# Kernel optimization log

Measured on AMD Instinct MI355X. Metric: run time of the kernel, lower is better.

## Reference

```python
import jax, jax.numpy as jnp
import numpy as np


def apply_rope(x):
    # x: [B, T, H, D]
    T, D = x.shape[1], x.shape[3]
    inv_freq = 1.0 / (10000.0 ** (jnp.arange(0, D, 2, dtype=jnp.float32) / D))  # [D/2]
    t = jnp.arange(T, dtype=jnp.float32)
    freqs = jnp.outer(t, inv_freq)  # [T, D/2]
    sin_f = jnp.sin(freqs)[None, :, None, :]
    cos_f = jnp.cos(freqs)[None, :, None, :]
    x1, x2 = jnp.split(x, 2, axis=-1)
    return jnp.concatenate([x1 * cos_f - x2 * sin_f, x1 * sin_f + x2 * cos_f], axis=-1)


def setup_inputs() -> dict:
    key = jax.random.key(0)
    ks = jax.random.split(key, 5)
    B, T, D = 8, 8192, 128
    s = 1.0 / np.sqrt(D)
    return {
        "x": jax.random.normal(ks[0], (B, T, D), dtype=jnp.float32),
        "Wq": jax.random.normal(ks[1], (D, D), dtype=jnp.float32) * s,
        "bq": jnp.zeros((D,), dtype=jnp.float32),
        "Wk": jax.random.normal(ks[2], (D, D), dtype=jnp.float32) * s,
        "bk": jnp.zeros((D,), dtype=jnp.float32),
        "Wv": jax.random.normal(ks[3], (D, D), dtype=jnp.float32) * s,
        "bv": jnp.zeros((D,), dtype=jnp.float32),
        "Wo": jax.random.normal(ks[4], (D, D), dtype=jnp.float32) * s,
        "bo": jnp.zeros((D,), dtype=jnp.float32),
    }


def reference(x, Wq, bq, Wk, bk, Wv, bv, Wo, bo):
    n_heads = 8
    B, T, d_model = x.shape
    head_dim = d_model // n_heads

    q = (x @ Wq + bq).reshape(B, T, n_heads, head_dim)
    k = (x @ Wk + bk).reshape(B, T, n_heads, head_dim)
    v = (x @ Wv + bv).reshape(B, T, n_heads, head_dim)

    q = jax.nn.elu(apply_rope(q)) + 1.0
    k = jax.nn.elu(apply_rope(k)) + 1.0

    # non-causal linear attention: context = sum_t k_t v_t^T per head
    context = jnp.einsum("bthd,bthe->bhde", k, v)            # [B,H,Dh,Dh]
    out = jnp.einsum("bthd,bhde->bthe", q, context)           # [B,T,H,Dh]
    k_sum = jnp.sum(k, axis=1)                                  # [B,H,Dh]
    z = 1.0 / (jnp.einsum("bthd,bhd->bth", q, k_sum) + 1e-6)  # [B,T,H]
    out = out * z[..., None]

    out = out.reshape(B, T, d_model)
    return out @ Wo + bo
```

## Files before the change

kernel.cpp:

```cpp
#include <hip/hip_runtime.h>
#include <hip/hip_bf16.h>


typedef __attribute__((ext_vector_type(8))) short short8;
typedef __attribute__((ext_vector_type(4))) float floatx4;

#define DEV __device__ __forceinline__
#define MFMA __builtin_amdgcn_mfma_f32_16x16x32_bf16

DEV unsigned short bfh(float f) {
  unsigned int x = __float_as_uint(f);
  x += 0x7fffu + ((x >> 16) & 1u);
  return (unsigned short)(x >> 16);
}
DEV float bfdec(unsigned short u) { return __uint_as_float(((unsigned int)u) << 16); }
DEV void splitf(float f, unsigned short& h, unsigned short& l) {
  h = bfh(f);
  l = bfh(f - bfdec(h));
}
DEV void split8(const float* p, short8& h8, short8& l8) {
  float4 a = *(const float4*)p;
  float4 b = *(const float4*)(p + 4);
  float v[8] = {a.x, a.y, a.z, a.w, b.x, b.y, b.z, b.w};
  union { short8 s; unsigned short u[8]; } H, L;
#pragma unroll
  for (int i = 0; i < 8; ++i) splitf(v[i], H.u[i], L.u[i]);
  h8 = H.s; l8 = L.s;
}

DEV void xpose_frag(floatx4 m0, floatx4 m1, int lane16, int quad,
                    short8& hi, short8& lo) {
  union { short8 s; unsigned short u[8]; } H, L;
#pragma unroll
  for (int j = 0; j < 8; ++j) {
    int srcLane = lane16 + (((quad & 1) * 2 + (j >> 2)) << 4);
    float vA = __shfl(m0[j & 3], srcLane, 64);
    float vB = __shfl(m1[j & 3], srcLane, 64);
    float v = (quad < 2) ? vA : vB;
    splitf(v, H.u[j], L.u[j]);
  }
  hi = H.s; lo = L.s;
}

__global__ void k_prep(const float* __restrict__ Wq, const float* __restrict__ Wk,
                       const float* __restrict__ Wv, const float* __restrict__ Wo,
                       unsigned short* __restrict__ WTh, unsigned short* __restrict__ WTl,
                       float* __restrict__ ctxz) {
  int gid = blockIdx.x * 256 + threadIdx.x;
  if (gid < 8192) {
    int mat = gid >> 11, r = gid & 2047, n = r >> 4, k0 = (r & 15) * 8;
    const float* W = (mat == 0) ? Wq : (mat == 1) ? Wk : (mat == 2) ? Wv : Wo;
    union { uint4 q; unsigned short u[8]; } oh, ol;
#pragma unroll
    for (int i = 0; i < 8; ++i) splitf(W[(size_t)(k0 + i) * 128 + n], oh.u[i], ol.u[i]);
    *(uint4*)&WTh[mat * 16384 + n * 128 + k0] = oh.q;
    *(uint4*)&WTl[mat * 16384 + n * 128 + k0] = ol.q;
  } else if (gid < 8192 + 17408) {
    ctxz[gid - 8192] = 0.0f;
  }
}

DEV void stage_rope64(int tid, int t0, float rc[64][9], float rs[64][9]) {
#pragma unroll
  for (int p = 0; p < 2; ++p) {
    int idx = tid + p * 256;
    int r = idx >> 3, j = idx & 7;
    float invf = 1.0f / powf(10000.0f, (float)j * 0.125f);
    float s, c;
    sincosf((float)(t0 + r) * invf, &s, &c);
    rc[r][j] = c; rs[r][j] = s;
  }
}

__global__ __launch_bounds__(256, 2) void k_qkv_ctx(
    const float* __restrict__ x,
    const unsigned short* __restrict__ WTh, const unsigned short* __restrict__ WTl,
    const float* __restrict__ bq, const float* __restrict__ bk, const float* __restrict__ bv,
    float* __restrict__ ctx, float* __restrict__ ksum,
    unsigned short* __restrict__ qws) {
  __shared__ float rc[64][9], rs[64][9];
  const int tid = threadIdx.x;
  const int row0 = blockIdx.x * 64;
  const int b = row0 >> 13;
  const int t0 = row0 & 8191;

  stage_rope64(tid, t0, rc, rs);
  __syncthreads();

  const int l = tid & 63, w = tid >> 6;
  const int lane16 = l & 15, quad = l >> 4;

  floatx4 acc[6][4];
#pragma unroll
  for (int i = 0; i < 6; ++i)
#pragma unroll
    for (int j = 0; j < 4; ++j) acc[i][j] = (floatx4){0.f, 0.f, 0.f, 0.f};

#pragma unroll
  for (int ks = 0; ks < 4; ++ks) {
    short8 afh[4], afl[4];
#pragma unroll
    for (int mt = 0; mt < 4; ++mt)
      split8(x + (size_t)(row0 + mt * 16 + lane16) * 128 + ks * 32 + quad * 8, afh[mt], afl[mt]);
#pragma unroll
    for (int nt = 0; nt < 6; ++nt) {
      int mat = nt >> 1;
      size_t woff = (size_t)mat * 16384 +
                    (size_t)(w * 32 + (nt & 1) * 16 + lane16) * 128 + ks * 32 + quad * 8;
      short8 bh = *(const short8*)(WTh + woff);
      short8 bl = *(const short8*)(WTl + woff);
#pragma unroll
      for (int mt = 0; mt < 4; ++mt) {
        acc[nt][mt] = MFMA(afh[mt], bh, acc[nt][mt], 0, 0, 0);
        acc[nt][mt] = MFMA(afl[mt], bh, acc[nt][mt], 0, 0, 0);
        acc[nt][mt] = MFMA(afh[mt], bl, acc[nt][mt], 0, 0, 0);
      }
    }
  }

#pragma unroll
  for (int nt = 0; nt < 6; ++nt) {
    int col = w * 32 + (nt & 1) * 16 + lane16;
    int mat = nt >> 1;
    float bias = (mat == 0) ? bq[col] : (mat == 1) ? bk[col] : bv[col];
#pragma unroll
    for (int mt = 0; mt < 4; ++mt)
#pragma unroll
      for (int r = 0; r < 4; ++r) acc[nt][mt][r] += bias;
  }

  {
    const int d = lane16, j = d & 7;
#pragma unroll
    for (int mt = 0; mt < 4; ++mt) {
      float cc[4], ss[4];
#pragma unroll
      for (int r = 0; r < 4; ++r) {
        int tl = mt * 16 + quad * 4 + r;
        cc[r] = rc[tl][j]; ss[r] = rs[tl][j];
      }
#pragma unroll
      for (int nt = 0; nt < 4; ++nt) {
#pragma unroll
        for (int r = 0; r < 4; ++r) {
          float v = acc[nt][mt][r];
          float p = __shfl_xor(v, 8);
          float nv = (d < 8) ? (v * cc[r] - p * ss[r]) : (p * ss[r] + v * cc[r]);
          acc[nt][mt][r] = (nv > 0.f) ? (nv + 1.f) : __expf(nv);
        }
      }
    }
  }

#pragma unroll
  for (int kt = 0; kt < 2; ++kt) {
    float s = 0.f;
#pragma unroll
    for (int mt = 0; mt < 4; ++mt)
#pragma unroll
      for (int r = 0; r < 4; ++r) s += acc[2 + kt][mt][r];
    s += __shfl_xor(s, 16);
    s += __shfl_xor(s, 32);
    if (l < 16) atomicAdd(&ksum[(b * 8 + w * 2 + kt) * 16 + lane16], s);
  }

#pragma unroll
  for (int qt = 0; qt < 2; ++qt) {
    int h = w * 2 + qt;
#pragma unroll
    for (int mt = 0; mt < 4; ++mt)
#pragma unroll
      for (int r = 0; r < 4; ++r)
        qws[(size_t)(row0 + mt * 16 + quad * 4 + r) * 128 + h * 16 + lane16] =
            bfh(acc[qt][mt][r]);
  }

#pragma unroll
  for (int hl = 0; hl < 2; ++hl) {
    int h = w * 2 + hl;
    floatx4 c = (floatx4){0.f, 0.f, 0.f, 0.f};
#pragma unroll
    for (int ks2 = 0; ks2 < 2; ++ks2) {
      short8 kh, kl, vh, vl;
      xpose_frag(acc[2 + hl][ks2 * 2], acc[2 + hl][ks2 * 2 + 1], lane16, quad, kh, kl);
      xpose_frag(acc[4 + hl][ks2 * 2], acc[4 + hl][ks2 * 2 + 1], lane16, quad, vh, vl);
      c = MFMA(kh, vh, c, 0, 0, 0);
      c = MFMA(kl, vh, c, 0, 0, 0);
      c = MFMA(kh, vl, c, 0, 0, 0);
    }
#pragma unroll
    for (int r = 0; r < 4; ++r)
      atomicAdd(&ctx[((size_t)(b * 8 + h) * 16 + quad * 4 + r) * 16 + lane16], c[r]);
  }
}

__global__ __launch_bounds__(256, 2) void k_apply_out(
    const unsigned short* __restrict__ qws,
    const unsigned short* __restrict__ WToh, const unsigned short* __restrict__ WTol,
    const float* __restrict__ bo,
    const float* __restrict__ ctx, const float* __restrict__ ksum,
    float* __restrict__ out) {
  __shared__ unsigned short CTh[8 * 16 * 40], CTl[8 * 16 * 40];
  __shared__ float ksumS[128], boS[128];
  const int tid = threadIdx.x;
  const int row0 = blockIdx.x * 128;
  const int b = row0 >> 13;

  if (tid < 128) {
    int h = tid >> 4, e = tid & 15, p = h & 1;
    unsigned int base = (h * 16 + e) * 40;
    union { uint4 q; unsigned int u[4]; } z0; z0.u[0] = z0.u[1] = z0.u[2] = z0.u[3] = 0;
    *(uint4*)&CTh[base + (1 - p) * 16] = z0.q;
    *(uint4*)&CTh[base + (1 - p) * 16 + 8] = z0.q;
    *(uint4*)&CTl[base + (1 - p) * 16] = z0.q;
    *(uint4*)&CTl[base + (1 - p) * 16 + 8] = z0.q;
    const float* cp = ctx + (size_t)(b * 8 + h) * 256 + e;
    union { uint4 q; unsigned short u[8]; } ch, cl;
#pragma unroll
    for (int d = 0; d < 8; ++d) splitf(cp[d * 16], ch.u[d], cl.u[d]);
    *(uint4*)&CTh[base + p * 16] = ch.q;
    *(uint4*)&CTl[base + p * 16] = cl.q;
#pragma unroll
    for (int d = 0; d < 8; ++d) splitf(cp[(8 + d) * 16], ch.u[d], cl.u[d]);
    *(uint4*)&CTh[base + p * 16 + 8] = ch.q;
    *(uint4*)&CTl[base + p * 16 + 8] = cl.q;
  } else {
    int t2 = tid - 128;
    ksumS[t2] = ksum[b * 128 + t2];
    boS[t2] = bo[t2];
  }
  __syncthreads();

  const int l = tid & 63, w = tid >> 6;
  const int lane16 = l & 15, quad = l >> 4;

  floatx4 of[2][8];
  short8 qf[2][4];
  float ziP[2][4];

#pragma unroll
  for (int mt2 = 0; mt2 < 2; ++mt2) {
    int trow = row0 + w * 32 + mt2 * 16 + lane16;
#pragma unroll
    for (int hp = 0; hp < 4; ++hp)
      qf[mt2][hp] = *(const short8*)&qws[(size_t)trow * 128 + hp * 32 + quad * 8];
#pragma unroll
    for (int hp = 0; hp < 4; ++hp) {
      union { short8 s8; unsigned short u[8]; } qq; qq.s8 = qf[mt2][hp];
      float s = 0.f;
#pragma unroll
      for (int jj = 0; jj < 8; ++jj)
        s += bfdec(qq.u[jj]) * ksumS[hp * 32 + quad * 8 + jj];
      s += __shfl_xor(s, 16);
      ziP[mt2][hp] = 1.0f / (s + 1e-6f);
    }
#pragma unroll
    for (int h = 0; h < 8; ++h) {
      int ca = (h * 16 + lane16) * 40 + quad * 8;
      short8 avh = *(const short8*)&CTh[ca];
      short8 avl = *(const short8*)&CTl[ca];
      floatx4 o = (floatx4){0.f, 0.f, 0.f, 0.f};
      o = MFMA(avh, qf[mt2][h >> 1], o, 0, 0, 0);
      o = MFMA(avl, qf[mt2][h >> 1], o, 0, 0, 0);
      float zz = __shfl(ziP[mt2][h >> 1], ((h & 1) << 5) + lane16, 64);
#pragma unroll
      for (int r = 0; r < 4; ++r) of[mt2][h][r] = o[r] * zz;
    }
  }

  short8 oah[2][4], oal[2][4];
#pragma unroll
  for (int mt2 = 0; mt2 < 2; ++mt2)
#pragma unroll
    for (int ksx = 0; ksx < 4; ++ksx)
      xpose_frag(of[mt2][ksx * 2], of[mt2][ksx * 2 + 1], lane16, quad, oah[mt2][ksx], oal[mt2][ksx]);

  floatx4 oacc[2][8];
#pragma unroll
  for (int i = 0; i < 2; ++i)
#pragma unroll
    for (int j = 0; j < 8; ++j) oacc[i][j] = (floatx4){0.f, 0.f, 0.f, 0.f};

#pragma unroll
  for (int nt = 0; nt < 8; ++nt) {
#pragma unroll
    for (int ks = 0; ks < 4; ++ks) {
      size_t off = (size_t)(nt * 16 + lane16) * 128 + ks * 32 + quad * 8;
      short8 wbh = *(const short8*)(WToh + off);
      short8 wbl = *(const short8*)(WTol + off);
#pragma unroll
      for (int mt2 = 0; mt2 < 2; ++mt2) {
        oacc[mt2][nt] = MFMA(oah[mt2][ks], wbh, oacc[mt2][nt], 0, 0, 0);
        oacc[mt2][nt] = MFMA(oal[mt2][ks], wbh, oacc[mt2][nt], 0, 0, 0);
        oacc[mt2][nt] = MFMA(oah[mt2][ks], wbl, oacc[mt2][nt], 0, 0, 0);
      }
    }
  }

#pragma unroll
  for (int nt = 0; nt < 8; ++nt) {
    int oc = nt * 16 + lane16;
    float bb = boS[oc];
#pragma unroll
    for (int mt2 = 0; mt2 < 2; ++mt2)
#pragma unroll
      for (int r = 0; r < 4; ++r) {
        int t = row0 + w * 32 + mt2 * 16 + quad * 4 + r;
        out[(size_t)t * 128 + oc] = oacc[mt2][nt][r] + bb;
      }
  }
}

extern "C" void kernel_launch(void* const* d_in, const int* in_sizes, int n_in,
                              void* d_out, int out_size, void* d_ws, size_t ws_size,
                              hipStream_t stream) {
  const float* x  = (const float*)d_in[0];
  const float* Wq = (const float*)d_in[1];
  const float* bq = (const float*)d_in[2];
  const float* Wk = (const float*)d_in[3];
  const float* bk = (const float*)d_in[4];
  const float* Wv = (const float*)d_in[5];
  const float* bv = (const float*)d_in[6];
  const float* Wo = (const float*)d_in[7];
  const float* bo = (const float*)d_in[8];
  float* out = (float*)d_out;

  unsigned short* qws = (unsigned short*)d_ws;
  unsigned short* WTh = qws + 8388608;
  unsigned short* WTl = WTh + 65536;
  float* ctx  = (float*)(WTl + 65536);
  float* ksum = ctx + 16384;

  k_prep<<<100, 256, 0, stream>>>(Wq, Wk, Wv, Wo, WTh, WTl, ctx);
  k_qkv_ctx<<<1024, 256, 0, stream>>>(x, WTh, WTl, bq, bk, bv, ctx, ksum, qws);
  k_apply_out<<<512, 256, 0, stream>>>(qws, WTh + 3 * 16384, WTl + 3 * 16384,
                                       bo, ctx, ksum, out);
}
```

Before: 172.3 us.

## Fold context into Wo per batch and stage split x in LDS with 512 threads

```diff
diff --git a/kernel.cpp b/kernel.cpp
--- a/kernel.cpp
+++ b/kernel.cpp
@@ -43,56 +43,62 @@
 }
 
 __global__ void k_prep(const float* __restrict__ Wq, const float* __restrict__ Wk,
-                       const float* __restrict__ Wv, const float* __restrict__ Wo,
+                       const float* __restrict__ Wv,
                        unsigned short* __restrict__ WTh, unsigned short* __restrict__ WTl,
                        float* __restrict__ ctxz) {
   int gid = blockIdx.x * 256 + threadIdx.x;
-  if (gid < 8192) {
+  if (gid < 6144) {
     int mat = gid >> 11, r = gid & 2047, n = r >> 4, k0 = (r & 15) * 8;
-    const float* W = (mat == 0) ? Wq : (mat == 1) ? Wk : (mat == 2) ? Wv : Wo;
+    const float* W = (mat == 0) ? Wq : (mat == 1) ? Wk : Wv;
     union { uint4 q; unsigned short u[8]; } oh, ol;
 #pragma unroll
     for (int i = 0; i < 8; ++i) splitf(W[(size_t)(k0 + i) * 128 + n], oh.u[i], ol.u[i]);
     *(uint4*)&WTh[mat * 16384 + n * 128 + k0] = oh.q;
     *(uint4*)&WTl[mat * 16384 + n * 128 + k0] = ol.q;
-  } else if (gid < 8192 + 17408) {
-    ctxz[gid - 8192] = 0.0f;
-  }
-}
-
-DEV void stage_rope64(int tid, int t0, float rc[64][9], float rs[64][9]) {
-#pragma unroll
-  for (int p = 0; p < 2; ++p) {
-    int idx = tid + p * 256;
-    int r = idx >> 3, j = idx & 7;
-    float invf = 1.0f / powf(10000.0f, (float)j * 0.125f);
-    float s, c;
-    sincosf((float)(t0 + r) * invf, &s, &c);
-    rc[r][j] = c; rs[r][j] = s;
-  }
-}
-
-__global__ __launch_bounds__(256, 2) void k_qkv_ctx(
+  } else if (gid < 6144 + 17408) {
+    ctxz[gid - 6144] = 0.0f;
+  }
+}
+
+__global__ __launch_bounds__(512) void k_qkv(
     const float* __restrict__ x,
     const unsigned short* __restrict__ WTh, const unsigned short* __restrict__ WTl,
     const float* __restrict__ bq, const float* __restrict__ bk, const float* __restrict__ bv,
     float* __restrict__ ctx, float* __restrict__ ksum,
     unsigned short* __restrict__ qws) {
+  __shared__ unsigned short xh[64 * 136], xl[64 * 136];
   __shared__ float rc[64][9], rs[64][9];
   const int tid = threadIdx.x;
   const int row0 = blockIdx.x * 64;
   const int b = row0 >> 13;
   const int t0 = row0 & 8191;
 
-  stage_rope64(tid, t0, rc, rs);
+  {
+    int r = tid >> 3, j = tid & 7;
+    float invf = 1.0f / powf(10000.0f, (float)j * 0.125f);
+    float s, c;
+    sincosf((float)(t0 + r) * invf, &s, &c);
+    rc[r][j] = c; rs[r][j] = s;
+  }
+  {
+    int r = tid >> 3, cg = (tid & 7) * 16;
+    const float* xp = x + (size_t)(row0 + r) * 128 + cg;
+    short8 h0, l0, h1, l1;
+    split8(xp, h0, l0);
+    split8(xp + 8, h1, l1);
+    *(short8*)&xh[r * 136 + cg] = h0;
+    *(short8*)&xh[r * 136 + cg + 8] = h1;
+    *(short8*)&xl[r * 136 + cg] = l0;
+    *(short8*)&xl[r * 136 + cg + 8] = l1;
+  }
   __syncthreads();
 
   const int l = tid & 63, w = tid >> 6;
   const int lane16 = l & 15, quad = l >> 4;
 
-  floatx4 acc[6][4];
-#pragma unroll
-  for (int i = 0; i < 6; ++i)
+  floatx4 acc[3][4];
+#pragma unroll
+  for (int i = 0; i < 3; ++i)
 #pragma unroll
     for (int j = 0; j < 4; ++j) acc[i][j] = (floatx4){0.f, 0.f, 0.f, 0.f};
 
@@ -100,33 +106,35 @@
   for (int ks = 0; ks < 4; ++ks) {
     short8 afh[4], afl[4];
 #pragma unroll
-    for (int mt = 0; mt < 4; ++mt)
-      split8(x + (size_t)(row0 + mt * 16 + lane16) * 128 + ks * 32 + quad * 8, afh[mt], afl[mt]);
-#pragma unroll
-    for (int nt = 0; nt < 6; ++nt) {
-      int mat = nt >> 1;
+    for (int mt = 0; mt < 4; ++mt) {
+      int off = (mt * 16 + lane16) * 136 + ks * 32 + quad * 8;
+      afh[mt] = *(const short8*)&xh[off];
+      afl[mt] = *(const short8*)&xl[off];
+    }
+#pragma unroll
+    for (int mat = 0; mat < 3; ++mat) {
       size_t woff = (size_t)mat * 16384 +
-                    (size_t)(w * 32 + (nt & 1) * 16 + lane16) * 128 + ks * 32 + quad * 8;
+                    (size_t)(w * 16 + lane16) * 128 + ks * 32 + quad * 8;
       short8 bh = *(const short8*)(WTh + woff);
       short8 bl = *(const short8*)(WTl + woff);
 #pragma unroll
       for (int mt = 0; mt < 4; ++mt) {
-        acc[nt][mt] = MFMA(afh[mt], bh, acc[nt][mt], 0, 0, 0);
-        acc[nt][mt] = MFMA(afl[mt], bh, acc[nt][mt], 0, 0, 0);
-        acc[nt][mt] = MFMA(afh[mt], bl, acc[nt][mt], 0, 0, 0);
-      }
-    }
-  }
-
-#pragma unroll
-  for (int nt = 0; nt < 6; ++nt) {
-    int col = w * 32 + (nt & 1) * 16 + lane16;
-    int mat = nt >> 1;
-    float bias = (mat == 0) ? bq[col] : (mat == 1) ? bk[col] : bv[col];
-#pragma unroll
-    for (int mt = 0; mt < 4; ++mt)
-#pragma unroll
-      for (int r = 0; r < 4; ++r) acc[nt][mt][r] += bias;
+        acc[mat][mt] = MFMA(afh[mt], bh, acc[mat][mt], 0, 0, 0);
+        acc[mat][mt] = MFMA(afl[mt], bh, acc[mat][mt], 0, 0, 0);
+        acc[mat][mt] = MFMA(afh[mt], bl, acc[mat][mt], 0, 0, 0);
+      }
+    }
+  }
+
+  {
+    int col = w * 16 + lane16;
+    float bias[3] = {bq[col], bk[col], bv[col]};
+#pragma unroll
+    for (int mat = 0; mat < 3; ++mat)
+#pragma unroll
+      for (int mt = 0; mt < 4; ++mt)
+#pragma unroll
+        for (int r = 0; r < 4; ++r) acc[mat][mt][r] += bias[mat];
   }
 
   {
@@ -140,140 +148,113 @@
         cc[r] = rc[tl][j]; ss[r] = rs[tl][j];
       }
 #pragma unroll
-      for (int nt = 0; nt < 4; ++nt) {
+      for (int mat = 0; mat < 2; ++mat) {
 #pragma unroll
         for (int r = 0; r < 4; ++r) {
-          float v = acc[nt][mt][r];
+          float v = acc[mat][mt][r];
           float p = __shfl_xor(v, 8);
           float nv = (d < 8) ? (v * cc[r] - p * ss[r]) : (p * ss[r] + v * cc[r]);
-          acc[nt][mt][r] = (nv > 0.f) ? (nv + 1.f) : __expf(nv);
+          acc[mat][mt][r] = (nv > 0.f) ? (nv + 1.f) : __expf(nv);
         }
       }
     }
   }
 
-#pragma unroll
-  for (int kt = 0; kt < 2; ++kt) {
+  {
     float s = 0.f;
 #pragma unroll
     for (int mt = 0; mt < 4; ++mt)
 #pragma unroll
-      for (int r = 0; r < 4; ++r) s += acc[2 + kt][mt][r];
+      for (int r = 0; r < 4; ++r) s += acc[1][mt][r];
     s += __shfl_xor(s, 16);
     s += __shfl_xor(s, 32);
-    if (l < 16) atomicAdd(&ksum[(b * 8 + w * 2 + kt) * 16 + lane16], s);
-  }
-
-#pragma unroll
-  for (int qt = 0; qt < 2; ++qt) {
-    int h = w * 2 + qt;
-#pragma unroll
-    for (int mt = 0; mt < 4; ++mt)
-#pragma unroll
-      for (int r = 0; r < 4; ++r)
-        qws[(size_t)(row0 + mt * 16 + quad * 4 + r) * 128 + h * 16 + lane16] =
-            bfh(acc[qt][mt][r]);
-  }
-
-#pragma unroll
-  for (int hl = 0; hl < 2; ++hl) {
-    int h = w * 2 + hl;
+    if (l < 16) atomicAdd(&ksum[(b * 8 + w) * 16 + lane16], s);
+  }
+
+#pragma unroll
+  for (int mt = 0; mt < 4; ++mt)
+#pragma unroll
+    for (int r = 0; r < 4; ++r)
+      qws[(size_t)(row0 + mt * 16 + quad * 4 + r) * 128 + w * 16 + lane16] =
+          bfh(acc[0][mt][r]);
+
+  {
     floatx4 c = (floatx4){0.f, 0.f, 0.f, 0.f};
 #pragma unroll
     for (int ks2 = 0; ks2 < 2; ++ks2) {
       short8 kh, kl, vh, vl;
-      xpose_frag(acc[2 + hl][ks2 * 2], acc[2 + hl][ks2 * 2 + 1], lane16, quad, kh, kl);
-      xpose_frag(acc[4 + hl][ks2 * 2], acc[4 + hl][ks2 * 2 + 1], lane16, quad, vh, vl);
+      xpose_frag(acc[1][ks2 * 2], acc[1][ks2 * 2 + 1], lane16, quad, kh, kl);
+      xpose_frag(acc[2][ks2 * 2], acc[2][ks2 * 2 + 1], lane16, quad, vh, vl);
       c = MFMA(kh, vh, c, 0, 0, 0);
       c = MFMA(kl, vh, c, 0, 0, 0);
       c = MFMA(kh, vl, c, 0, 0, 0);
     }
 #pragma unroll
     for (int r = 0; r < 4; ++r)
-      atomicAdd(&ctx[((size_t)(b * 8 + h) * 16 + quad * 4 + r) * 16 + lane16], c[r]);
-  }
-}
-
-__global__ __launch_bounds__(256, 2) void k_apply_out(
+      atomicAdd(&ctx[((size_t)(b * 8 + w) * 16 + quad * 4 + r) * 16 + lane16], c[r]);
+  }
+}
+
+__global__ void k_mprep(const float* __restrict__ Wo, const float* __restrict__ ctx,
+                        unsigned short* __restrict__ MTh, unsigned short* __restrict__ MTl) {
+  int gid = blockIdx.x * 256 + threadIdx.x;
+  int b = gid >> 11, r = gid & 2047, oc = r >> 4, qcg = r & 15;
+  int h = qcg >> 1, d0 = (qcg & 1) * 8;
+  const float* C = ctx + (size_t)(b * 8 + h) * 256;
+  float m[8] = {0.f, 0.f, 0.f, 0.f, 0.f, 0.f, 0.f, 0.f};
+#pragma unroll 4
+  for (int e = 0; e < 16; ++e) {
+    float wv = Wo[(size_t)(h * 16 + e) * 128 + oc];
+#pragma unroll
+    for (int i = 0; i < 8; ++i) m[i] += C[(d0 + i) * 16 + e] * wv;
+  }
+  union { uint4 q; unsigned short u[8]; } oh, ol;
+#pragma unroll
+  for (int i = 0; i < 8; ++i) splitf(m[i], oh.u[i], ol.u[i]);
+  *(uint4*)&MTh[(size_t)gid * 8] = oh.q;
+  *(uint4*)&MTl[(size_t)gid * 8] = ol.q;
+}
+
+__global__ __launch_bounds__(256) void k_zout(
     const unsigned short* __restrict__ qws,
-    const unsigned short* __restrict__ WToh, const unsigned short* __restrict__ WTol,
-    const float* __restrict__ bo,
-    const float* __restrict__ ctx, const float* __restrict__ ksum,
+    const unsigned short* __restrict__ MTh, const unsigned short* __restrict__ MTl,
+    const float* __restrict__ bo, const float* __restrict__ ksum,
     float* __restrict__ out) {
-  __shared__ unsigned short CTh[8 * 16 * 40], CTl[8 * 16 * 40];
   __shared__ float ksumS[128], boS[128];
   const int tid = threadIdx.x;
   const int row0 = blockIdx.x * 128;
   const int b = row0 >> 13;
 
-  if (tid < 128) {
-    int h = tid >> 4, e = tid & 15, p = h & 1;
-    unsigned int base = (h * 16 + e) * 40;
-    union { uint4 q; unsigned int u[4]; } z0; z0.u[0] = z0.u[1] = z0.u[2] = z0.u[3] = 0;
-    *(uint4*)&CTh[base + (1 - p) * 16] = z0.q;
-    *(uint4*)&CTh[base + (1 - p) * 16 + 8] = z0.q;
-    *(uint4*)&CTl[base + (1 - p) * 16] = z0.q;
-    *(uint4*)&CTl[base + (1 - p) * 16 + 8] = z0.q;
-    const float* cp = ctx + (size_t)(b * 8 + h) * 256 + e;
-    union { uint4 q; unsigned short u[8]; } ch, cl;
-#pragma unroll
-    for (int d = 0; d < 8; ++d) splitf(cp[d * 16], ch.u[d], cl.u[d]);
-    *(uint4*)&CTh[base + p * 16] = ch.q;
-    *(uint4*)&CTl[base + p * 16] = cl.q;
-#pragma unroll
-    for (int d = 0; d < 8; ++d) splitf(cp[(8 + d) * 16], ch.u[d], cl.u[d]);
-    *(uint4*)&CTh[base + p * 16 + 8] = ch.q;
-    *(uint4*)&CTl[base + p * 16 + 8] = cl.q;
-  } else {
-    int t2 = tid - 128;
-    ksumS[t2] = ksum[b * 128 + t2];
-    boS[t2] = bo[t2];
-  }
+  if (tid < 128) ksumS[tid] = ksum[b * 128 + tid];
+  else boS[tid - 128] = bo[tid - 128];
   __syncthreads();
 
   const int l = tid & 63, w = tid >> 6;
   const int lane16 = l & 15, quad = l >> 4;
-
-  floatx4 of[2][8];
-  short8 qf[2][4];
-  float ziP[2][4];
-
+  const unsigned short* MThb = MTh + (size_t)b * 16384;
+  const unsigned short* MTlb = MTl + (size_t)b * 16384;
+
+  short8 ah[2][4], al[2][4];
 #pragma unroll
   for (int mt2 = 0; mt2 < 2; ++mt2) {
     int trow = row0 + w * 32 + mt2 * 16 + lane16;
 #pragma unroll
-    for (int hp = 0; hp < 4; ++hp)
-      qf[mt2][hp] = *(const short8*)&qws[(size_t)trow * 128 + hp * 32 + quad * 8];
-#pragma unroll
-    for (int hp = 0; hp < 4; ++hp) {
-      union { short8 s8; unsigned short u[8]; } qq; qq.s8 = qf[mt2][hp];
+    for (int ks = 0; ks < 4; ++ks) {
+      union { short8 s8; unsigned short u[8]; } qq;
+      qq.s8 = *(const short8*)&qws[(size_t)trow * 128 + ks * 32 + quad * 8];
+      int kb = ks * 32 + quad * 8;
       float s = 0.f;
 #pragma unroll
-      for (int jj = 0; jj < 8; ++jj)
-        s += bfdec(qq.u[jj]) * ksumS[hp * 32 + quad * 8 + jj];
+      for (int j = 0; j < 8; ++j) s += bfdec(qq.u[j]) * ksumS[kb + j];
       s += __shfl_xor(s, 16);
-      ziP[mt2][hp] = 1.0f / (s + 1e-6f);
-    }
-#pragma unroll
-    for (int h = 0; h < 8; ++h) {
-      int ca = (h * 16 + lane16) * 40 + quad * 8;
-      short8 avh = *(const short8*)&CTh[ca];
-      short8 avl = *(const short8*)&CTl[ca];
-      floatx4 o = (floatx4){0.f, 0.f, 0.f, 0.f};
-      o = MFMA(avh, qf[mt2][h >> 1], o, 0, 0, 0);
-      o = MFMA(avl, qf[mt2][h >> 1], o, 0, 0, 0);
-      float zz = __shfl(ziP[mt2][h >> 1], ((h & 1) << 5) + lane16, 64);
-#pragma unroll
-      for (int r = 0; r < 4; ++r) of[mt2][h][r] = o[r] * zz;
-    }
-  }
-
-  short8 oah[2][4], oal[2][4];
-#pragma unroll
-  for (int mt2 = 0; mt2 < 2; ++mt2)
-#pragma unroll
-    for (int ksx = 0; ksx < 4; ++ksx)
-      xpose_frag(of[mt2][ksx * 2], of[mt2][ksx * 2 + 1], lane16, quad, oah[mt2][ksx], oal[mt2][ksx]);
+      float z = 1.0f / (s + 1e-6f);
+      union { short8 s8; unsigned short u[8]; } H, L;
+#pragma unroll
+      for (int j = 0; j < 8; ++j) splitf(bfdec(qq.u[j]) * z, H.u[j], L.u[j]);
+      ah[mt2][ks] = H.s8;
+      al[mt2][ks] = L.s8;
+    }
+  }
 
   floatx4 oacc[2][8];
 #pragma unroll
@@ -286,13 +267,13 @@
 #pragma unroll
     for (int ks = 0; ks < 4; ++ks) {
       size_t off = (size_t)(nt * 16 + lane16) * 128 + ks * 32 + quad * 8;
-      short8 wbh = *(const short8*)(WToh + off);
-      short8 wbl = *(const short8*)(WTol + off);
+      short8 wbh = *(const short8*)(MThb + off);
+      short8 wbl = *(const short8*)(MTlb + off);
 #pragma unroll
       for (int mt2 = 0; mt2 < 2; ++mt2) {
-        oacc[mt2][nt] = MFMA(oah[mt2][ks], wbh, oacc[mt2][nt], 0, 0, 0);
-        oacc[mt2][nt] = MFMA(oal[mt2][ks], wbh, oacc[mt2][nt], 0, 0, 0);
-        oacc[mt2][nt] = MFMA(oah[mt2][ks], wbl, oacc[mt2][nt], 0, 0, 0);
+        oacc[mt2][nt] = MFMA(ah[mt2][ks], wbh, oacc[mt2][nt], 0, 0, 0);
+        oacc[mt2][nt] = MFMA(al[mt2][ks], wbh, oacc[mt2][nt], 0, 0, 0);
+        oacc[mt2][nt] = MFMA(ah[mt2][ks], wbl, oacc[mt2][nt], 0, 0, 0);
       }
     }
   }
@@ -327,12 +308,14 @@
 
   unsigned short* qws = (unsigned short*)d_ws;
   unsigned short* WTh = qws + 8388608;
-  unsigned short* WTl = WTh + 65536;
-  float* ctx  = (float*)(WTl + 65536);
+  unsigned short* WTl = WTh + 49152;
+  float* ctx  = (float*)(WTl + 49152);
   float* ksum = ctx + 16384;
-
-  k_prep<<<100, 256, 0, stream>>>(Wq, Wk, Wv, Wo, WTh, WTl, ctx);
-  k_qkv_ctx<<<1024, 256, 0, stream>>>(x, WTh, WTl, bq, bk, bv, ctx, ksum, qws);
-  k_apply_out<<<512, 256, 0, stream>>>(qws, WTh + 3 * 16384, WTl + 3 * 16384,
-                                       bo, ctx, ksum, out);
-}
+  unsigned short* MTh = (unsigned short*)(ksum + 1024);
+  unsigned short* MTl = MTh + 131072;
+
+  k_prep<<<92, 256, 0, stream>>>(Wq, Wk, Wv, WTh, WTl, ctx);
+  k_qkv<<<1024, 512, 0, stream>>>(x, WTh, WTl, bq, bk, bv, ctx, ksum, qws);
+  k_mprep<<<64, 256, 0, stream>>>(Wo, ctx, MTh, MTl);
+  k_zout<<<512, 256, 0, stream>>>(qws, MTh, MTl, bo, ksum, out);
+}
```

Result: no change. 171.6 us (-0.4%).
